# Optimization experiments

Measured on AMD Instinct MI355X. Metric: run time of the kernel, lower is better.

## Reference

```python
import jax, jax.numpy as jnp
import numpy as np

# Static config (matches init_kwargs)
B, H, W, C = 16, 56, 56, 512
WS, SHIFT, NH = 7, 3, 16
HD = C // NH
N = WS * WS
NW = (H // WS) * (W // WS)
SCALE = HD ** -0.5
EPS = 1e-5


def _relative_position_index():
    coords = np.stack(np.meshgrid(np.arange(WS), np.arange(WS), indexing='ij'))  # (2,WS,WS)
    flat = coords.reshape(2, -1)                       # (2,N)
    rel = flat[:, :, None] - flat[:, None, :]          # (2,N,N)
    rel = rel.transpose(1, 2, 0).astype(np.int64)
    rel[..., 0] += WS - 1
    rel[..., 1] += WS - 1
    rel[..., 0] *= 2 * WS - 1
    return rel.sum(-1)                                 # (N,N)


def _window_partition_np(x):
    # x: (H,W) numpy -> (NW, N)
    return x.reshape(H // WS, WS, W // WS, WS).transpose(0, 2, 1, 3).reshape(-1, N)


def _attn_mask():
    img = np.zeros((H, W))
    cnt = 0
    for hs in (slice(0, -WS), slice(-WS, -SHIFT), slice(-SHIFT, None)):
        for ws_ in (slice(0, -WS), slice(-WS, -SHIFT), slice(-SHIFT, None)):
            img[hs, ws_] = cnt
            cnt += 1
    mw = _window_partition_np(img)                     # (NW, N)
    diff = mw[:, None, :] - mw[:, :, None]             # (NW, N, N)
    return np.where(diff != 0, -100.0, 0.0).astype(np.float32)


REL_IDX = jnp.asarray(_relative_position_index())
ATTN_MASK = jnp.asarray(_attn_mask())


def window_partition(x):
    # x: (B,H,W,C) -> (B*NW, N, C)
    x = x.reshape(B, H // WS, WS, W // WS, WS, C)
    return x.transpose(0, 1, 3, 2, 4, 5).reshape(-1, N, C)


def window_reverse(w):
    # w: (B*NW, N, C) -> (B,H,W,C)
    x = w.reshape(B, H // WS, W // WS, WS, WS, C)
    return x.transpose(0, 1, 3, 2, 4, 5).reshape(B, H, W, C)


def layer_norm(x, g, b):
    m = x.mean(-1, keepdims=True)
    v = jnp.mean((x - m) ** 2, axis=-1, keepdims=True)
    return (x - m) * jax.lax.rsqrt(v + EPS) * g + b


def before_cross_attention(x, g, b):
    # x: (B, L, C) -> shifted windows (B*NW, N, C)
    x = layer_norm(x, g, b).reshape(B, H, W, C)
    x = jnp.roll(x, (-SHIFT, -SHIFT), axis=(1, 2))
    return window_partition(x)


def get_qkv(x, Wqkv, bqkv):
    # x: (B_, N, C); Wqkv: (C, 3C)
    qkv = (x @ Wqkv + bqkv).reshape(-1, N, 3, NH, HD).transpose(2, 0, 3, 1, 4)
    return qkv[0], qkv[1], qkv[2]  # each (B_, NH, N, HD)


def setup_inputs() -> dict:
    key = jax.random.key(0)
    ks = jax.random.split(key, 10)
    s = 0.02
    return {
        'rescaled': jax.random.normal(ks[0], (B, H * W, C), jnp.float32),
        'rescaler': jax.random.normal(ks[1], (B, H * W, C), jnp.float32),
        'gamma_a': jnp.ones((C,), jnp.float32),
        'beta_a': jnp.zeros((C,), jnp.float32),
        'gamma_b': jnp.ones((C,), jnp.float32),
        'beta_b': jnp.zeros((C,), jnp.float32),
        'Wqkv_a': jax.random.normal(ks[2], (C, 3 * C), jnp.float32) * s,
        'bqkv_a': jnp.zeros((3 * C,), jnp.float32),
        'Wqkv_b': jax.random.normal(ks[3], (C, 3 * C), jnp.float32) * s,
        'bqkv_b': jnp.zeros((3 * C,), jnp.float32),
        'rpb_table': jax.random.normal(ks[4], ((2 * WS - 1) ** 2, NH), jnp.float32) * s,
        'Wproj': jax.random.normal(ks[5], (C, C), jnp.float32) * s,
        'bproj': jnp.zeros((C,), jnp.float32),
    }


def reference(rescaled, rescaler, gamma_a, beta_a, gamma_b, beta_b,
              Wqkv_a, bqkv_a, Wqkv_b, bqkv_b, rpb_table, Wproj, bproj):
    # norm + shift + window partition for both streams
    xw = before_cross_attention(rescaled, gamma_a, beta_a)   # (B*NW, N, C)
    yw = before_cross_attention(rescaler, gamma_b, beta_b)

    q_a, k_a, v_a = get_qkv(xw, Wqkv_a, bqkv_a)  # rescaled stream
    q_b, k_b, v_b = get_qkv(yw, Wqkv_b, bqkv_b)  # rescaler stream
    # same_key_query=False: q from rescaler, k & v from rescaled
    q, k, v = q_b * SCALE, k_a, v_a

    attn = jnp.einsum('bhnd,bhmd->bhnm', q, k)               # (B*NW, NH, N, N)
    rpb = rpb_table[REL_IDX.reshape(-1)].reshape(N, N, NH).transpose(2, 0, 1)
    attn = attn + rpb[None]
    attn = attn.reshape(B, NW, NH, N, N) + ATTN_MASK[None, :, None]
    attn = jax.nn.softmax(attn.reshape(-1, NH, N, N), axis=-1)

    out = jnp.einsum('bhnm,bhmd->bhnd', attn, v)             # (B*NW, NH, N, HD)
    out = out.transpose(0, 2, 1, 3).reshape(-1, N, C)
    out = out @ Wproj + bproj

    # window reverse + un-shift, back to (B, L, C)
    x = window_reverse(out)
    x = jnp.roll(x, (SHIFT, SHIFT), axis=(1, 2))
    return x.reshape(B, H * W, C)
```

## Files before the change

kernel.cpp:

```cpp
#include <hip/hip_runtime.h>
#include <hip/hip_bf16.h>


typedef short bf16x8 __attribute__((ext_vector_type(8)));
typedef float f32x4 __attribute__((ext_vector_type(4)));
typedef unsigned short u16;

#define MTOT 50176
#define SCALE_ 0.17677669529663687f

__device__ __forceinline__ u16 f2bf(float f) {
    __hip_bfloat16 h = __float2bfloat16(f);
    return *reinterpret_cast<u16*>(&h);
}
__device__ __forceinline__ float bf2f(u16 u) {
    union { unsigned int i; float f; } t; t.i = ((unsigned int)u) << 16; return t.f;
}

#define ASYNC_COPY16(g, l)                                                      \
    __builtin_amdgcn_global_load_lds((__attribute__((address_space(1))) void*)(g), \
                                     (__attribute__((address_space(3))) void*)(l), 16, 0, 0)

__global__ __launch_bounds__(256) void wconv_kernel(
    const float* __restrict__ Wqkv_a, const float* __restrict__ Wqkv_b,
    const float* __restrict__ Wproj, u16* __restrict__ Wt)
{
    const int idx = blockIdx.x * 256 + threadIdx.x;
    const int r = idx >> 9;
    const int k = idx & 511;
    float val;
    if (r < 512)       val = Wqkv_b[k * 1536 + r];
    else if (r < 1536) val = Wqkv_a[k * 1536 + r];
    else               val = Wproj[k * 512 + (r - 1536)];
    Wt[idx] = f2bf(val);
}

__global__ __launch_bounds__(256) void build_bias_kernel(
    const float* __restrict__ rpb, float* __restrict__ bias)
{
    const int blk = blockIdx.x;
    const int mid = blk >> 4, head = blk & 15;
    const int whq = (mid >> 1) & 1, wwq = mid & 1;
    for (int t = threadIdx.x; t < 4096; t += 256) {
        const int i = t >> 6, j = t & 63;
        float v;
        if (i < 49 && j < 49) {
            const int ih = i / 7, iw = i - ih * 7;
            const int jh = j / 7, jw = j - jh * 7;
            v = rpb[((ih - jh + 6) * 13 + (iw - jw + 6)) * 16 + head];
            const int li = (whq ? (ih < 4 ? 1 : 2) : 0) * 3 + (wwq ? (iw < 4 ? 1 : 2) : 0);
            const int lj = (whq ? (jh < 4 ? 1 : 2) : 0) * 3 + (wwq ? (jw < 4 ? 1 : 2) : 0);
            if (li != lj) v -= 100.0f;
        } else {
            v = -3.0e38f;
        }
        bias[(size_t)blk * 4096 + t] = v;
    }
}

__device__ __forceinline__ void ln_one(
    const float* __restrict__ src, const float* __restrict__ g,
    const float* __restrict__ bt, u16* __restrict__ dst, int lane)
{
    const float4 v0 = *(const float4*)(src + lane * 8);
    const float4 v1 = *(const float4*)(src + lane * 8 + 4);
    float s = v0.x + v0.y + v0.z + v0.w + v1.x + v1.y + v1.z + v1.w;
    float q = v0.x*v0.x + v0.y*v0.y + v0.z*v0.z + v0.w*v0.w
            + v1.x*v1.x + v1.y*v1.y + v1.z*v1.z + v1.w*v1.w;
#pragma unroll
    for (int o = 32; o >= 1; o >>= 1) { s += __shfl_xor(s, o); q += __shfl_xor(q, o); }
    const float mean = s * (1.0f / 512.0f);
    const float rstd = rsqrtf(q * (1.0f / 512.0f) - mean * mean + 1e-5f);
    const float4 g0 = *(const float4*)(g + lane * 8);
    const float4 g1 = *(const float4*)(g + lane * 8 + 4);
    const float4 b0 = *(const float4*)(bt + lane * 8);
    const float4 b1 = *(const float4*)(bt + lane * 8 + 4);
    u16 o8[8];
    o8[0] = f2bf((v0.x - mean) * rstd * g0.x + b0.x);
    o8[1] = f2bf((v0.y - mean) * rstd * g0.y + b0.y);
    o8[2] = f2bf((v0.z - mean) * rstd * g0.z + b0.z);
    o8[3] = f2bf((v0.w - mean) * rstd * g0.w + b0.w);
    o8[4] = f2bf((v1.x - mean) * rstd * g1.x + b1.x);
    o8[5] = f2bf((v1.y - mean) * rstd * g1.y + b1.y);
    o8[6] = f2bf((v1.z - mean) * rstd * g1.z + b1.z);
    o8[7] = f2bf((v1.w - mean) * rstd * g1.w + b1.w);
    int4 pk;
    pk.x = (int)(((unsigned)o8[1] << 16) | o8[0]);
    pk.y = (int)(((unsigned)o8[3] << 16) | o8[2]);
    pk.z = (int)(((unsigned)o8[5] << 16) | o8[4]);
    pk.w = (int)(((unsigned)o8[7] << 16) | o8[6]);
    *(int4*)(dst + lane * 8) = pk;
}

__global__ __launch_bounds__(256) void ln_window_kernel(
    const float* __restrict__ xa, const float* __restrict__ xb,
    const float* __restrict__ ga, const float* __restrict__ bea,
    const float* __restrict__ gb, const float* __restrict__ beb,
    u16* __restrict__ xw, u16* __restrict__ yw)
{
    const int wave = threadIdx.x >> 6, lane = threadIdx.x & 63;
    const int row = blockIdx.x * 4 + wave;
    const int win = row / 49, n = row - win * 49;
    const int b = win >> 6, wi = win & 63;
    const int wh = wi >> 3, ww = wi & 7;
    const int ih = n / 7, iw = n - ih * 7;
    int h = wh * 7 + ih + 3; if (h >= 56) h -= 56;
    int w = ww * 7 + iw + 3; if (w >= 56) w -= 56;
    const size_t src = ((size_t)b * 3136 + (size_t)h * 56 + w) * 512;
    const size_t dst = (size_t)row * 512;
    ln_one(xa + src, ga, bea, xw + dst, lane);
    ln_one(xb + src, gb, beb, yw + dst, lane);
}

#define GEMM8_MAIN()                                                            \
    __shared__ __align__(16) u16 As[128 * 64];                                  \
    __shared__ __align__(16) u16 Bs[256 * 64];                                  \
    const int tid = threadIdx.x;                                                \
    const int lane = tid & 63;                                                  \
    const int wv = tid >> 6;                                                    \
    const int wm = wv >> 2, wn = wv & 3;                                        \
    const int rowl = lane & 15, kg = lane >> 4;                                 \
    const int sw = rowl & 7;                                                    \
    f32x4 acc[4][4];                                                            \
    for (int i = 0; i < 4; ++i)                                                 \
        for (int j = 0; j < 4; ++j)                                             \
            acc[i][j] = (f32x4){0.f, 0.f, 0.f, 0.f};                            \
    const int srow = tid >> 3;                                                  \
    const int clog = (tid & 7) ^ (srow & 7);                                    \
    const u16* Ab = Asrc + (size_t)(mt * 128 + srow) * 512 + clog * 8;          \
    const u16* Bb = Bsrc + (size_t)srow * 512 + clog * 8;                       \
    char* AsD = (char*)As + tid * 16;                                           \
    char* BsD = (char*)Bs + tid * 16;                                           \
    for (int kt = 0; kt < 8; ++kt) {                                            \
        const int k0 = kt * 64;                                                 \
        _Pragma("unroll")                                                       \
        for (int r = 0; r < 2; ++r)                                             \
            ASYNC_COPY16(Ab + (size_t)r * 64 * 512 + k0, AsD + r * 8192);       \
        _Pragma("unroll")                                                       \
        for (int r = 0; r < 4; ++r)                                             \
            ASYNC_COPY16(Bb + (size_t)r * 64 * 512 + k0, BsD + r * 8192);       \
        asm volatile("s_waitcnt vmcnt(0)" ::: "memory");                        \
        __syncthreads();                                                        \
        _Pragma("unroll")                                                       \
        for (int kk = 0; kk < 2; ++kk) {                                        \
            const int kch = kg + kk * 4;                                        \
            const int sco = (kch ^ sw) * 8;                                     \
            bf16x8 af[4], bfr[4];                                               \
            _Pragma("unroll")                                                   \
            for (int i = 0; i < 4; ++i)                                         \
                af[i] = *(const bf16x8*)(As + (wm * 64 + i * 16 + rowl) * 64 + sco); \
            _Pragma("unroll")                                                   \
            for (int j = 0; j < 4; ++j)                                         \
                bfr[j] = *(const bf16x8*)(Bs + (wn * 64 + j * 16 + rowl) * 64 + sco); \
            _Pragma("unroll")                                                   \
            for (int i = 0; i < 4; ++i) {                                       \
                _Pragma("unroll")                                               \
                for (int j = 0; j < 4; ++j)                                     \
                    acc[i][j] = __builtin_amdgcn_mfma_f32_16x16x32_bf16(        \
                        af[i], bfr[j], acc[i][j], 0, 0, 0);                     \
            }                                                                   \
        }                                                                       \
        __syncthreads();                                                        \
    }

__global__ __launch_bounds__(512) void gemm_qkv_kernel(
    const u16* __restrict__ xw, const u16* __restrict__ yw,
    const u16* __restrict__ Wt,
    const float* __restrict__ bqkv_a, const float* __restrict__ bqkv_b,
    u16* __restrict__ qb, u16* __restrict__ kb, u16* __restrict__ vb)
{
    const int bid = blockIdx.x;
    const int swz = (bid & 7) * 294 + (bid >> 3);
    const int nt = swz % 6;
    const int mt = swz / 6;
    const u16* Asrc = (nt < 2) ? yw : xw;
    const u16* Bsrc = Wt + (size_t)(nt * 256) * 512;
    GEMM8_MAIN()

    u16* dst; const float* bvec; bool isq = false;
    if (nt < 2)      { dst = qb; bvec = bqkv_b; isq = true; }
    else if (nt < 4) { dst = kb; bvec = bqkv_a; }
    else             { dst = vb; bvec = bqkv_a; }
#pragma unroll
    for (int j = 0; j < 4; ++j) {
        const int col = nt * 256 + wn * 64 + j * 16 + rowl;
        const float bias_ = bvec[col];
        const int pcol = col & 511;
#pragma unroll
        for (int i = 0; i < 4; ++i) {
#pragma unroll
            for (int rr = 0; rr < 4; ++rr) {
                const int row = mt * 128 + wm * 64 + i * 16 + kg * 4 + rr;
                float val = acc[i][j][rr] + bias_;
                if (isq) val *= SCALE_;
                dst[(size_t)row * 512 + pcol] = f2bf(val);
            }
        }
    }
}

__global__ __launch_bounds__(512) void gemm_proj_kernel(
    const u16* __restrict__ attn_out, const u16* __restrict__ WtProj,
    const float* __restrict__ bproj, float* __restrict__ out)
{
    const int bid = blockIdx.x;
    const int swz = (bid & 7) * 98 + (bid >> 3);
    const int nt = swz & 1;
    const int mt = swz >> 1;
    const u16* Asrc = attn_out;
    const u16* Bsrc = WtProj + (size_t)(nt * 256) * 512;
    GEMM8_MAIN()

#pragma unroll
    for (int j = 0; j < 4; ++j) {
        const int col = nt * 256 + wn * 64 + j * 16 + rowl;
        const float bias_ = bproj[col];
#pragma unroll
        for (int i = 0; i < 4; ++i) {
#pragma unroll
            for (int rr = 0; rr < 4; ++rr) {
                const int row = mt * 128 + wm * 64 + i * 16 + kg * 4 + rr;
                const int win = row / 49;
                const int nw = row - win * 49;
                const int b = win >> 6, wi = win & 63;
                const int wh = wi >> 3, ww = wi & 7;
                const int ih = nw / 7, iw = nw - ih * 7;
                int h = wh * 7 + ih + 3; if (h >= 56) h -= 56;
                int w = ww * 7 + iw + 3; if (w >= 56) w -= 56;
                out[((size_t)b * 3136 + (size_t)h * 56 + w) * 512 + col] =
                    acc[i][j][rr] + bias_;
            }
        }
    }
}

__global__ __launch_bounds__(256) void attn_kernel(
    const u16* __restrict__ qb, const u16* __restrict__ kb,
    const u16* __restrict__ vb, const float* __restrict__ bias,
    u16* __restrict__ attn_out)
{
    __shared__ __align__(16) u16 VT[32 * 64];
    __shared__ __align__(16) u16 P[64 * 64];
    const int tid = threadIdx.x;
    const int wh_id = blockIdx.x;
    const int win = wh_id >> 4, head = wh_id & 15;
    const int lane = tid & 63, wvi = tid >> 6;
    const int rowl = lane & 15, kg = lane >> 4;
    const size_t base = (size_t)win * 49 * 512 + head * 32;

    {
        const int j = tid >> 2, d0 = (tid & 3) * 8;
        const bf16x8 v8 = *(const bf16x8*)(vb + base + (size_t)j * 512 + d0);
        const int cj = j >> 3, je = j & 7;
#pragma unroll
        for (int m = 0; m < 8; ++m) {
            const int d = d0 + m;
            VT[d * 64 + ((cj ^ (d & 7)) * 8) + je] = (u16)v8[m];
        }
    }

    const bf16x8 aq = *(const bf16x8*)(qb + base + (size_t)(wvi * 16 + rowl) * 512 + kg * 8);
    f32x4 accS[4];
#pragma unroll
    for (int j = 0; j < 4; ++j) {
        const bf16x8 bk = *(const bf16x8*)(kb + base + (size_t)(j * 16 + rowl) * 512 + kg * 8);
        accS[j] = __builtin_amdgcn_mfma_f32_16x16x32_bf16(
            aq, bk, (f32x4){0.f, 0.f, 0.f, 0.f}, 0, 0, 0);
    }

    const int wi = win & 63;
    const int mid = (((wi >> 3) == 7) ? 2 : 0) + (((wi & 7) == 7) ? 1 : 0);
    const float* bptr = bias + ((size_t)(mid * 16 + head) << 12);
#pragma unroll
    for (int j = 0; j < 4; ++j)
#pragma unroll
        for (int r = 0; r < 4; ++r)
            accS[j][r] += bptr[(wvi * 16 + kg * 4 + r) * 64 + j * 16 + rowl];

    float rinv[4];
#pragma unroll
    for (int r = 0; r < 4; ++r) {
        float m = fmaxf(fmaxf(accS[0][r], accS[1][r]), fmaxf(accS[2][r], accS[3][r]));
#pragma unroll
        for (int o = 1; o <= 8; o <<= 1) m = fmaxf(m, __shfl_xor(m, o));
        float s = 0.f;
#pragma unroll
        for (int j = 0; j < 4; ++j) {
            accS[j][r] = __expf(accS[j][r] - m);
            s += accS[j][r];
        }
#pragma unroll
        for (int o = 1; o <= 8; o <<= 1) s += __shfl_xor(s, o);
        rinv[r] = __frcp_rn(s);
    }

#pragma unroll
    for (int j = 0; j < 4; ++j) {
        const int c = j * 2 + (rowl >> 3);
#pragma unroll
        for (int r = 0; r < 4; ++r) {
            const int row = wvi * 16 + kg * 4 + r;
            P[row * 64 + ((c ^ (row & 7)) * 8) + (rowl & 7)] = f2bf(accS[j][r]);
        }
    }

    __syncthreads();

    f32x4 accO[2];
#pragma unroll
    for (int dt = 0; dt < 2; ++dt) {
        accO[dt] = (f32x4){0.f, 0.f, 0.f, 0.f};
#pragma unroll
        for (int kb_ = 0; kb_ < 2; ++kb_) {
            const int prow = wvi * 16 + rowl;
            const int ca = kb_ * 4 + kg;
            const bf16x8 ap = *(const bf16x8*)(P + prow * 64 + ((ca ^ (prow & 7)) * 8));
            const int vd = dt * 16 + rowl;
            const bf16x8 bv = *(const bf16x8*)(VT + vd * 64 + ((ca ^ (vd & 7)) * 8));
            accO[dt] = __builtin_amdgcn_mfma_f32_16x16x32_bf16(ap, bv, accO[dt], 0, 0, 0);
        }
    }

#pragma unroll
    for (int dt = 0; dt < 2; ++dt) {
#pragma unroll
        for (int r = 0; r < 4; ++r) {
            const int i = wvi * 16 + kg * 4 + r;
            if (i < 49)
                attn_out[base + (size_t)i * 512 + dt * 16 + rowl] =
                    f2bf(accO[dt][r] * rinv[r]);
        }
    }
}

extern "C" void kernel_launch(void* const* d_in, const int* in_sizes, int n_in,
                              void* d_out, int out_size, void* d_ws, size_t ws_size,
                              hipStream_t stream) {
    (void)in_sizes; (void)n_in; (void)out_size; (void)ws_size;
    const float* rescaled = (const float*)d_in[0];
    const float* rescaler = (const float*)d_in[1];
    const float* gamma_a  = (const float*)d_in[2];
    const float* beta_a   = (const float*)d_in[3];
    const float* gamma_b  = (const float*)d_in[4];
    const float* beta_b   = (const float*)d_in[5];
    const float* Wqkv_a   = (const float*)d_in[6];
    const float* bqkv_a   = (const float*)d_in[7];
    const float* Wqkv_b   = (const float*)d_in[8];
    const float* bqkv_b   = (const float*)d_in[9];
    const float* rpb      = (const float*)d_in[10];
    const float* Wproj    = (const float*)d_in[11];
    const float* bproj    = (const float*)d_in[12];
    float* out = (float*)d_out;

    char* ws = (char*)d_ws;
    const size_t SZ = (size_t)MTOT * 512 * 2;
    u16* xw = (u16*)ws;
    u16* yw = (u16*)(ws + SZ);
    u16* qb = (u16*)(ws + 2 * SZ);
    u16* kb = (u16*)(ws + 3 * SZ);
    u16* vb = (u16*)(ws + 4 * SZ);
    u16* Wt = (u16*)(ws + 5 * SZ);
    float* bias = (float*)(ws + 5 * SZ + 2097152);
    u16* attn_out = xw;

    wconv_kernel<<<4096, 256, 0, stream>>>(Wqkv_a, Wqkv_b, Wproj, Wt);
    build_bias_kernel<<<64, 256, 0, stream>>>(rpb, bias);
    ln_window_kernel<<<MTOT / 4, 256, 0, stream>>>(
        rescaled, rescaler, gamma_a, beta_a, gamma_b, beta_b, xw, yw);
    gemm_qkv_kernel<<<2352, 512, 0, stream>>>(
        xw, yw, Wt, bqkv_a, bqkv_b, qb, kb, vb);
    attn_kernel<<<16384, 256, 0, stream>>>(qb, kb, vb, bias, attn_out);
    gemm_proj_kernel<<<784, 512, 0, stream>>>(
        attn_out, Wt + (size_t)1536 * 512, bproj, out);
}
```

Baseline: 521.1 us.

## Double-buffer GEMM K-tiles and transpose attention bias for vector loads

The shared GEMM main loop now uses two LDS buffers with 32-wide K tiles. The async global-to-LDS copy of the next tile is issued before the MFMAs on the current tile, so global loads overlap compute instead of stalling every iteration. The swizzle is adjusted for the narrower 32-element rows. Separately, the attention bias table is stored transposed so each lane reads its four bias values with one 16-byte load instead of four strided scalar loads. Risks include more loop iterations and barriers per K and possible LDS bank conflicts from the new swizzle.

```diff
diff --git a/kernel.cpp b/kernel.cpp
--- a/kernel.cpp
+++ b/kernel.cpp
@@ -36,17 +36,17 @@
 }
 
 __global__ __launch_bounds__(256) void build_bias_kernel(
-    const float* __restrict__ rpb, float* __restrict__ bias)
+    const float* __restrict__ rpb, float* __restrict__ biasT)
 {
     const int blk = blockIdx.x;
     const int mid = blk >> 4, head = blk & 15;
     const int whq = (mid >> 1) & 1, wwq = mid & 1;
     for (int t = threadIdx.x; t < 4096; t += 256) {
-        const int i = t >> 6, j = t & 63;
+        const int col = t >> 6, row = t & 63;
         float v;
-        if (i < 49 && j < 49) {
-            const int ih = i / 7, iw = i - ih * 7;
-            const int jh = j / 7, jw = j - jh * 7;
+        if (row < 49 && col < 49) {
+            const int ih = row / 7, iw = row - ih * 7;
+            const int jh = col / 7, jw = col - jh * 7;
             v = rpb[((ih - jh + 6) * 13 + (iw - jw + 6)) * 16 + head];
             const int li = (whq ? (ih < 4 ? 1 : 2) : 0) * 3 + (wwq ? (iw < 4 ? 1 : 2) : 0);
             const int lj = (whq ? (jh < 4 ? 1 : 2) : 0) * 3 + (wwq ? (jw < 4 ? 1 : 2) : 0);
@@ -54,7 +54,7 @@
         } else {
             v = -3.0e38f;
         }
-        bias[(size_t)blk * 4096 + t] = v;
+        biasT[(size_t)blk * 4096 + t] = v;
     }
 }
 
@@ -112,54 +112,57 @@
     ln_one(xb + src, gb, beb, yw + dst, lane);
 }
 
-#define GEMM8_MAIN()                                                            \
-    __shared__ __align__(16) u16 As[128 * 64];                                  \
-    __shared__ __align__(16) u16 Bs[256 * 64];                                  \
+#define GEMM8P_MAIN()                                                           \
+    __shared__ __align__(16) u16 As[2][128 * 32];                               \
+    __shared__ __align__(16) u16 Bs[2][256 * 32];                               \
     const int tid = threadIdx.x;                                                \
     const int lane = tid & 63;                                                  \
     const int wv = tid >> 6;                                                    \
     const int wm = wv >> 2, wn = wv & 3;                                        \
     const int rowl = lane & 15, kg = lane >> 4;                                 \
-    const int sw = rowl & 7;                                                    \
+    const int fsw = (rowl >> 1) & 3;               \
     f32x4 acc[4][4];                                                            \
     for (int i = 0; i < 4; ++i)                                                 \
         for (int j = 0; j < 4; ++j)                                             \
             acc[i][j] = (f32x4){0.f, 0.f, 0.f, 0.f};                            \
-    const int srow = tid >> 3;                                                  \
-    const int clog = (tid & 7) ^ (srow & 7);                                    \
-    const u16* Ab = Asrc + (size_t)(mt * 128 + srow) * 512 + clog * 8;          \
-    const u16* Bb = Bsrc + (size_t)srow * 512 + clog * 8;                       \
-    char* AsD = (char*)As + tid * 16;                                           \
-    char* BsD = (char*)Bs + tid * 16;                                           \
-    for (int kt = 0; kt < 8; ++kt) {                                            \
-        const int k0 = kt * 64;                                                 \
+    const int srow = tid >> 2;                                      \
+    const int scol = ((tid & 3) ^ ((tid >> 3) & 3)) * 8;      \
+    const u16* Ab  = Asrc + (size_t)(mt * 128 + srow) * 512 + scol;             \
+    const u16* Bb0 = Bsrc + (size_t)srow * 512 + scol;                          \
+    const u16* Bb1 = Bsrc + (size_t)(128 + srow) * 512 + scol;                  \
+                                        \
+    ASYNC_COPY16(Ab,  (char*)&As[0][0] + tid * 16);                             \
+    ASYNC_COPY16(Bb0, (char*)&Bs[0][0] + tid * 16);                             \
+    ASYNC_COPY16(Bb1, (char*)&Bs[0][0] + 8192 + tid * 16);                      \
+    asm volatile("s_waitcnt vmcnt(0)" ::: "memory");                            \
+    __syncthreads();                                                            \
+    for (int kt = 0; kt < 16; ++kt) {                                           \
+        const int cur = kt & 1, nxt = cur ^ 1;                                  \
+        if (kt < 15) {                                                          \
+            const int k1 = (kt + 1) * 32;                                       \
+            ASYNC_COPY16(Ab + k1,  (char*)&As[0][0] + nxt * 8192 + tid * 16);   \
+            ASYNC_COPY16(Bb0 + k1, (char*)&Bs[0][0] + nxt * 16384 + tid * 16);  \
+            ASYNC_COPY16(Bb1 + k1, (char*)&Bs[0][0] + nxt * 16384 + 8192 + tid * 16); \
+        }                                                                       \
+        const u16* Asb = &As[cur][0];                                           \
+        const u16* Bsb = &Bs[cur][0];                                           \
+        bf16x8 af[4], bfr[4];                                                   \
         _Pragma("unroll")                                                       \
-        for (int r = 0; r < 2; ++r)                                             \
-            ASYNC_COPY16(Ab + (size_t)r * 64 * 512 + k0, AsD + r * 8192);       \
+        for (int i = 0; i < 4; ++i)                                             \
+            af[i] = *(const bf16x8*)(Asb + (wm * 64 + i * 16 + rowl) * 32       \
+                                         + ((kg ^ fsw) * 8));                   \
         _Pragma("unroll")                                                       \
-        for (int r = 0; r < 4; ++r)                                             \
-            ASYNC_COPY16(Bb + (size_t)r * 64 * 512 + k0, BsD + r * 8192);       \
-        asm volatile("s_waitcnt vmcnt(0)" ::: "memory");                        \
-        __syncthreads();                                                        \
+        for (int j = 0; j < 4; ++j)                                             \
+            bfr[j] = *(const bf16x8*)(Bsb + (wn * 64 + j * 16 + rowl) * 32      \
+                                          + ((kg ^ fsw) * 8));                  \
         _Pragma("unroll")                                                       \
-        for (int kk = 0; kk < 2; ++kk) {                                        \
-            const int kch = kg + kk * 4;                                        \
-            const int sco = (kch ^ sw) * 8;                                     \
-            bf16x8 af[4], bfr[4];                                               \
-            _Pragma("unroll")                                                   \
-            for (int i = 0; i < 4; ++i)                                         \
-                af[i] = *(const bf16x8*)(As + (wm * 64 + i * 16 + rowl) * 64 + sco); \
+        for (int i = 0; i < 4; ++i) {                                           \
             _Pragma("unroll")                                                   \
             for (int j = 0; j < 4; ++j)                                         \
-                bfr[j] = *(const bf16x8*)(Bs + (wn * 64 + j * 16 + rowl) * 64 + sco); \
-            _Pragma("unroll")                                                   \
-            for (int i = 0; i < 4; ++i) {                                       \
-                _Pragma("unroll")                                               \
-                for (int j = 0; j < 4; ++j)                                     \
-                    acc[i][j] = __builtin_amdgcn_mfma_f32_16x16x32_bf16(        \
-                        af[i], bfr[j], acc[i][j], 0, 0, 0);                     \
-            }                                                                   \
+                acc[i][j] = __builtin_amdgcn_mfma_f32_16x16x32_bf16(            \
+                    af[i], bfr[j], acc[i][j], 0, 0, 0);                         \
         }                                                                       \
+        asm volatile("s_waitcnt vmcnt(0)" ::: "memory");                        \
         __syncthreads();                                                        \
     }
 
@@ -175,7 +178,7 @@
     const int mt = swz / 6;
     const u16* Asrc = (nt < 2) ? yw : xw;
     const u16* Bsrc = Wt + (size_t)(nt * 256) * 512;
-    GEMM8_MAIN()
+    GEMM8P_MAIN()
 
     u16* dst; const float* bvec; bool isq = false;
     if (nt < 2)      { dst = qb; bvec = bqkv_b; isq = true; }
@@ -209,7 +212,7 @@
     const int mt = swz >> 1;
     const u16* Asrc = attn_out;
     const u16* Bsrc = WtProj + (size_t)(nt * 256) * 512;
-    GEMM8_MAIN()
+    GEMM8P_MAIN()
 
 #pragma unroll
     for (int j = 0; j < 4; ++j) {
@@ -236,7 +239,7 @@
 
 __global__ __launch_bounds__(256) void attn_kernel(
     const u16* __restrict__ qb, const u16* __restrict__ kb,
-    const u16* __restrict__ vb, const float* __restrict__ bias,
+    const u16* __restrict__ vb, const float* __restrict__ biasT,
     u16* __restrict__ attn_out)
 {
     __shared__ __align__(16) u16 VT[32 * 64];
@@ -270,12 +273,14 @@
 
     const int wi = win & 63;
     const int mid = (((wi >> 3) == 7) ? 2 : 0) + (((wi & 7) == 7) ? 1 : 0);
-    const float* bptr = bias + ((size_t)(mid * 16 + head) << 12);
-#pragma unroll
-    for (int j = 0; j < 4; ++j)
+    const float* bptr = biasT + ((size_t)(mid * 16 + head) << 12);
+#pragma unroll
+    for (int j = 0; j < 4; ++j) {
+        const f32x4 bv4 = *(const f32x4*)(bptr + (j * 16 + rowl) * 64 + wvi * 16 + kg * 4);
 #pragma unroll
         for (int r = 0; r < 4; ++r)
-            accS[j][r] += bptr[(wvi * 16 + kg * 4 + r) * 64 + j * 16 + rowl];
+            accS[j][r] += bv4[r];
+    }
 
     float rinv[4];
 #pragma unroll
@@ -360,16 +365,16 @@
     u16* kb = (u16*)(ws + 3 * SZ);
     u16* vb = (u16*)(ws + 4 * SZ);
     u16* Wt = (u16*)(ws + 5 * SZ);
-    float* bias = (float*)(ws + 5 * SZ + 2097152);
+    float* biasT = (float*)(ws + 5 * SZ + 2097152);
     u16* attn_out = xw;
 
     wconv_kernel<<<4096, 256, 0, stream>>>(Wqkv_a, Wqkv_b, Wproj, Wt);
-    build_bias_kernel<<<64, 256, 0, stream>>>(rpb, bias);
+    build_bias_kernel<<<64, 256, 0, stream>>>(rpb, biasT);
     ln_window_kernel<<<MTOT / 4, 256, 0, stream>>>(
         rescaled, rescaler, gamma_a, beta_a, gamma_b, beta_b, xw, yw);
     gemm_qkv_kernel<<<2352, 512, 0, stream>>>(
         xw, yw, Wt, bqkv_a, bqkv_b, qb, kb, vb);
-    attn_kernel<<<16384, 256, 0, stream>>>(qb, kb, vb, bias, attn_out);
+    attn_kernel<<<16384, 256, 0, stream>>>(qb, kb, vb, biasT, attn_out);
     gemm_proj_kernel<<<784, 512, 0, stream>>>(
         attn_out, Wt + (size_t)1536 * 512, bproj, out);
 }
```

New measurement: 534.4 us. +2.5%, slower.
